# Kernel tuning notes

Hardware: AMD Instinct MI355X
Metric: run time of the kernel (lower is better)

The kernel has to match this reference:

```python
import jax, jax.numpy as jnp
import numpy as np

EPS = 1e-5
B, S, P = 2, 512, 4096
TD, SD, H, ED = 512, 384, 8, 32
HD = TD // H


def _ln(x, g, b):
    m = jnp.mean(x, axis=-1, keepdims=True)
    v = jnp.var(x, axis=-1, keepdims=True)
    return (x - m) * jax.lax.rsqrt(v + EPS) * g + b


def setup_inputs() -> dict:
    key = jax.random.key(0)
    ks = iter(jax.random.split(key, 24))

    def lin(din, dout):
        W = jax.random.normal(next(ks), (din, dout), jnp.float32) / np.sqrt(din)
        b = jnp.zeros((dout,), jnp.float32)
        return W, b

    Wq, bq = lin(TD, TD)
    Wk, bk = lin(SD, TD)
    Wv, bv = lin(SD, TD)
    Wo, bo = lin(TD, TD)
    W1, b1 = lin(TD, 4 * TD)
    W2, b2 = lin(4 * TD, TD)
    edge_emb = jax.random.normal(next(ks), (H, ED), jnp.float32)
    ep_w = jax.random.normal(next(ks), (ED,), jnp.float32) / np.sqrt(ED)
    ep_b = jnp.zeros((), jnp.float32)

    return dict(
        text_features=jax.random.normal(next(ks), (B, S, TD), jnp.float32),
        shape_features=jax.random.normal(next(ks), (B, P, SD), jnp.float32),
        tn_g=jnp.ones((TD,), jnp.float32), tn_b=jnp.zeros((TD,), jnp.float32),
        sn_g=jnp.ones((SD,), jnp.float32), sn_b=jnp.zeros((SD,), jnp.float32),
        Wq=Wq, bq=bq, Wk=Wk, bk=bk, Wv=Wv, bv=bv,
        edge_emb=edge_emb, ep_w=ep_w, ep_b=ep_b,
        Wo=Wo, bo=bo,
        on_g=jnp.ones((TD,), jnp.float32), on_b=jnp.zeros((TD,), jnp.float32),
        W1=W1, b1=b1, W2=W2, b2=b2,
        fn_g=jnp.ones((TD,), jnp.float32), fn_b=jnp.zeros((TD,), jnp.float32),
    )


def reference(text_features, shape_features, tn_g, tn_b, sn_g, sn_b,
              Wq, bq, Wk, bk, Wv, bv, edge_emb, ep_w, ep_b, Wo, bo,
              on_g, on_b, W1, b1, W2, b2, fn_g, fn_b):
    b, n, _ = text_features.shape
    tn = _ln(text_features, tn_g, tn_b)
    sn = _ln(shape_features, sn_g, sn_b)
    residual = text_features

    # [b, h, n, d] projections
    q = (tn @ Wq + bq).reshape(b, n, H, HD).transpose(0, 2, 1, 3)
    k = (sn @ Wk + bk).reshape(b, -1, H, HD).transpose(0, 2, 1, 3)
    v = (sn @ Wv + bv).reshape(b, -1, H, HD).transpose(0, 2, 1, 3)

    scale = HD ** -0.5
    base_attn = jnp.einsum('bhid,bhjd->bhij', q, k) * scale  # [b,h,n,p]

    # edge_attn[:,h] = base_attn[:,h,:,:,None] * edge_emb[h]; then Linear(ED,1)+LeakyReLU.
    # Algebraically: score = leaky_relu(base_attn * (edge_emb @ ep_w) + ep_b)
    s = edge_emb @ ep_w  # [H] per-head scalar
    edge_scores = jax.nn.leaky_relu(base_attn * s[None, :, None, None] + ep_b, 0.2)

    attn = jax.nn.softmax(base_attn + edge_scores, axis=-1)
    out = jnp.einsum('bhij,bhjd->bhid', attn, v)
    out = out.transpose(0, 2, 1, 3).reshape(b, n, TD)
    out = out @ Wo + bo
    out = _ln(residual + out, on_g, on_b)

    ffn = jax.nn.gelu(out @ W1 + b1, approximate=False) @ W2 + b2
    out = _ln(out + ffn, fn_g, fn_b)
    return out, attn
```

## Files before the change

### kernel.cpp

```cpp
#include <hip/hip_runtime.h>
#include <math.h>

#define B_  2
#define S_  512
#define P_  4096
#define TD_ 512
#define SD_ 384
#define H_  8
#define HD_ 64
#define FF_ 2048

typedef _Float16 half8 __attribute__((ext_vector_type(8)));
typedef _Float16 half4 __attribute__((ext_vector_type(4)));
typedef float floatx4 __attribute__((ext_vector_type(4)));

__global__ __launch_bounds__(256) void wtrans_all_kernel(
    const float* __restrict__ s0p, const float* __restrict__ s1p,
    const float* __restrict__ s2p, const float* __restrict__ s3p,
    const float* __restrict__ s4p, const float* __restrict__ s5p,
    _Float16* __restrict__ d0p, _Float16* __restrict__ d1p,
    _Float16* __restrict__ d2p, _Float16* __restrict__ d3p,
    _Float16* __restrict__ d4p, _Float16* __restrict__ d5p)
{
    __shared__ float ts[32][33];
    int id = blockIdx.x;
    const float* src; _Float16* dst; int K, N, t, nlog;
    if (id < 256)       { src=s0p; dst=d0p; K=512;  N=512;  t=id;       nlog=4; }
    else if (id < 448)  { src=s1p; dst=d1p; K=384;  N=512;  t=id-256;   nlog=4; }
    else if (id < 640)  { src=s2p; dst=d2p; K=384;  N=512;  t=id-448;   nlog=4; }
    else if (id < 896)  { src=s3p; dst=d3p; K=512;  N=512;  t=id-640;   nlog=4; }
    else if (id < 1920) { src=s4p; dst=d4p; K=512;  N=2048; t=id-896;   nlog=6; }
    else                { src=s5p; dst=d5p; K=2048; N=512;  t=id-1920;  nlog=4; }
    int n0 = (t & ((1 << nlog) - 1)) << 5;
    int k0 = (t >> nlog) << 5;
    int tid = threadIdx.x;
#pragma unroll
    for (int i = 0; i < 4; ++i) {
        int e = i * 256 + tid;
        int kk = e >> 5, nn = e & 31;
        ts[kk][nn] = src[(size_t)(k0 + kk) * N + n0 + nn];
    }
    __syncthreads();
#pragma unroll
    for (int i = 0; i < 4; ++i) {
        int e = i * 256 + tid;
        int nn = e >> 5, kk = e & 31;
        dst[(size_t)(n0 + nn) * K + k0 + kk] = (_Float16)ts[kk][nn];
    }
}

__device__ __forceinline__ float2 block_sum2(float a, float b) {
    for (int off = 32; off > 0; off >>= 1) {
        a += __shfl_down(a, off);
        b += __shfl_down(b, off);
    }
    __shared__ float sa[8], sb[8];
    int w = threadIdx.x >> 6;
    if ((threadIdx.x & 63) == 0) { sa[w] = a; sb[w] = b; }
    __syncthreads();
    int nw = blockDim.x >> 6;
    float ta = 0.f, tb = 0.f;
    for (int i = 0; i < nw; ++i) { ta += sa[i]; tb += sb[i]; }
    __syncthreads();
    return make_float2(ta, tb);
}

__global__ __launch_bounds__(256) void ln_both_kernel(
    const float* __restrict__ text, const float* __restrict__ shape,
    const float* __restrict__ tn_g, const float* __restrict__ tn_b,
    const float* __restrict__ sn_g, const float* __restrict__ sn_b,
    _Float16* __restrict__ tn_h, _Float16* __restrict__ sn_h)
{
    int row = blockIdx.x;
    const float* xr; const float* g; const float* be; _Float16* yr; int D;
    if (row < 1024) {
        D = 512; xr = text + (size_t)row * 512; g = tn_g; be = tn_b;
        yr = tn_h + (size_t)row * 512;
    } else {
        int r2 = row - 1024;
        D = 384; xr = shape + (size_t)r2 * 384; g = sn_g; be = sn_b;
        yr = sn_h + (size_t)r2 * 384;
    }
    float s = 0.f, s2 = 0.f;
    for (int i = threadIdx.x; i < D; i += 256) {
        float v = xr[i]; s += v; s2 += v * v;
    }
    float2 r = block_sum2(s, s2);
    float mean = r.x / (float)D;
    float var  = r.y / (float)D - mean * mean;
    float rstd = rsqrtf(var + 1e-5f);
    for (int i = threadIdx.x; i < D; i += 256)
        yr[i] = (_Float16)((xr[i] - mean) * rstd * g[i] + be[i]);
}

__global__ __launch_bounds__(256) void ln_add_kernel(
    const float* __restrict__ a, const float* __restrict__ c, int np, int cstride,
    const float* __restrict__ g, const float* __restrict__ be,
    float* __restrict__ yf, _Float16* __restrict__ yh, int D)
{
    int row = blockIdx.x;
    const float* ar = a + (size_t)row * D;
    const float* cr = c + (size_t)row * D;
    float s = 0.f, s2 = 0.f;
    for (int i = threadIdx.x; i < D; i += 256) {
        float v = ar[i];
        for (int t = 0; t < np; ++t) v += cr[(size_t)t * cstride + i];
        s += v; s2 += v * v;
    }
    float2 rd = block_sum2(s, s2);
    float mean = rd.x / (float)D;
    float var  = rd.y / (float)D - mean * mean;
    float rstd = rsqrtf(var + 1e-5f);
    for (int i = threadIdx.x; i < D; i += 256) {
        float v = ar[i];
        for (int t = 0; t < np; ++t) v += cr[(size_t)t * cstride + i];
        float o = (v - mean) * rstd * g[i] + be[i];
        if (yf) yf[(size_t)row * D + i] = o;
        if (yh) yh[(size_t)row * D + i] = (_Float16)o;
    }
}

template<int ACT, int OUTF, int OUTH, int SPLITK>
__global__ __launch_bounds__(256) void gemm_f16_kernel(
    const _Float16* __restrict__ A, const _Float16* __restrict__ Bt,
    const float* __restrict__ bias, float* __restrict__ Cf,
    _Float16* __restrict__ Ch, int M, int N, int K)
{
    __shared__ _Float16 As[128 * 40];
    __shared__ _Float16 Bs[128 * 40];
    int tid = threadIdx.x;
    int bm = blockIdx.y * 128, bn = blockIdx.x * 128;
    int wave = tid >> 6, lane = tid & 63, quad = lane >> 4, r = lane & 15;
    int mh = (wave & 1) * 64, nh = (wave >> 1) * 64;

    floatx4 acc[4][4];
    floatx4 zz = {0.f, 0.f, 0.f, 0.f};
#pragma unroll
    for (int i = 0; i < 4; ++i)
#pragma unroll
        for (int j = 0; j < 4; ++j) acc[i][j] = zz;

    int srow = tid >> 2;
    int sko  = (tid & 3) * 8;

    int ksplit = (SPLITK > 1) ? blockIdx.z : 0;
    int kbeg = ksplit * (K / SPLITK);
    int kend = kbeg + K / SPLITK;

    for (int k0 = kbeg; k0 < kend; k0 += 32) {
#pragma unroll
        for (int i = 0; i < 2; ++i) {
            int row = i * 64 + srow;
            *(half8*)&As[row * 40 + sko] = *(const half8*)(A  + (size_t)(bm + row) * K + k0 + sko);
            *(half8*)&Bs[row * 40 + sko] = *(const half8*)(Bt + (size_t)(bn + row) * K + k0 + sko);
        }
        __syncthreads();
        half8 af[4], bf[4];
#pragma unroll
        for (int t = 0; t < 4; ++t) {
            af[t] = *(const half8*)&As[(mh + t * 16 + r) * 40 + quad * 8];
            bf[t] = *(const half8*)&Bs[(nh + t * 16 + r) * 40 + quad * 8];
        }
#pragma unroll
        for (int i = 0; i < 4; ++i)
#pragma unroll
            for (int j = 0; j < 4; ++j)
                acc[i][j] = __builtin_amdgcn_mfma_f32_16x16x32_f16(af[i], bf[j], acc[i][j], 0, 0, 0);
        __syncthreads();
    }

#pragma unroll
    for (int j = 0; j < 4; ++j) {
        int col = bn + nh + j * 16 + r;
        float bv = (SPLITK == 1 || ksplit == 0) ? bias[col] : 0.f;
#pragma unroll
        for (int i = 0; i < 4; ++i) {
#pragma unroll
            for (int g = 0; g < 4; ++g) {
                int row = bm + mh + i * 16 + quad * 4 + g;
                float v = acc[i][j][g] + bv;
                if (ACT) v = 0.5f * v * (1.0f + erff(v * 0.70710678118654752f));
                if (OUTF) Cf[(size_t)ksplit * M * N + (size_t)row * N + col] = v;
                if (OUTH) Ch[(size_t)row * N + col] = (_Float16)v;
            }
        }
    }
}

__global__ __launch_bounds__(256) void qkv_gemm_kernel(
    const _Float16* __restrict__ tn, const _Float16* __restrict__ sn,
    const _Float16* __restrict__ Wqt, const _Float16* __restrict__ Wkt,
    const _Float16* __restrict__ Wvt,
    const float* __restrict__ bq, const float* __restrict__ bk,
    const float* __restrict__ bv,
    _Float16* __restrict__ Qh, _Float16* __restrict__ Kh, _Float16* __restrict__ Vth)
{
    __shared__ _Float16 As[128 * 40];
    __shared__ _Float16 Bs[128 * 40];
    int by = blockIdx.y;
    const _Float16* A; const _Float16* Bt; const float* bias; _Float16* out;
    int K, bm, vt;
    if (by < 8)       { A = tn; Bt = Wqt; bias = bq; K = 512; bm = by * 128;        vt = 0; out = Qh;  }
    else if (by < 72) { A = sn; Bt = Wkt; bias = bk; K = 384; bm = (by - 8) * 128;  vt = 0; out = Kh;  }
    else              { A = sn; Bt = Wvt; bias = bv; K = 384; bm = (by - 72) * 128; vt = 1; out = Vth; }
    int bn = blockIdx.x * 128;
    int tid = threadIdx.x;
    int wave = tid >> 6, lane = tid & 63, quad = lane >> 4, r = lane & 15;
    int mh = (wave & 1) * 64, nh = (wave >> 1) * 64;

    floatx4 acc[4][4];
    floatx4 zz = {0.f, 0.f, 0.f, 0.f};
#pragma unroll
    for (int i = 0; i < 4; ++i)
#pragma unroll
        for (int j = 0; j < 4; ++j) acc[i][j] = zz;

    int srow = tid >> 2;
    int sko  = (tid & 3) * 8;

    for (int k0 = 0; k0 < K; k0 += 32) {
#pragma unroll
        for (int i = 0; i < 2; ++i) {
            int row = i * 64 + srow;
            *(half8*)&As[row * 40 + sko] = *(const half8*)(A  + (size_t)(bm + row) * K + k0 + sko);
            *(half8*)&Bs[row * 40 + sko] = *(const half8*)(Bt + (size_t)(bn + row) * K + k0 + sko);
        }
        __syncthreads();
        half8 af[4], bf[4];
#pragma unroll
        for (int t = 0; t < 4; ++t) {
            af[t] = *(const half8*)&As[(mh + t * 16 + r) * 40 + quad * 8];
            bf[t] = *(const half8*)&Bs[(nh + t * 16 + r) * 40 + quad * 8];
        }
#pragma unroll
        for (int i = 0; i < 4; ++i)
#pragma unroll
            for (int j = 0; j < 4; ++j)
                acc[i][j] = __builtin_amdgcn_mfma_f32_16x16x32_f16(af[i], bf[j], acc[i][j], 0, 0, 0);
        __syncthreads();
    }

#pragma unroll
    for (int j = 0; j < 4; ++j) {
        int col = bn + nh + j * 16 + r;
        float bvv = bias[col];
#pragma unroll
        for (int i = 0; i < 4; ++i) {
#pragma unroll
            for (int g = 0; g < 4; ++g) {
                int row = bm + mh + i * 16 + quad * 4 + g;
                float v = acc[i][j][g] + bvv;
                if (!vt) {
                    out[(size_t)row * 512 + col] = (_Float16)v;
                } else {
                    int bb = row >> 12, pp = row & 4095;
                    int hh = col >> 6,  dd = col & 63;
                    out[((size_t)((bb * 8 + hh) * 64 + dd)) * 4096 + pp] = (_Float16)v;
                }
            }
        }
    }
}

__global__ __launch_bounds__(256) void score_stats_kernel(
    const _Float16* __restrict__ Qh, const _Float16* __restrict__ Kh,
    const float* __restrict__ edge_emb, const float* __restrict__ ep_w,
    const float* __restrict__ ep_b, float2* __restrict__ part)
{
    __shared__ _Float16 Qs[128 * 72];
    __shared__ _Float16 Ks[128 * 72];
    __shared__ float mred[2][128];
    __shared__ float sred[2][128];
    int p0 = blockIdx.x * 128, s0 = blockIdx.y * 128;
    int bh = blockIdx.z, h = bh & 7, b = bh >> 3;
    int tid = threadIdx.x;
    int wave = tid >> 6, lane = tid & 63, quad = lane >> 4, r = lane & 15;
    int mh = (wave & 1) * 64, nh = (wave >> 1) * 64;

#pragma unroll
    for (int i = 0; i < 4; ++i) {
        int row = i * 32 + (tid >> 3);
        int ko  = (tid & 7) * 8;
        *(half8*)&Qs[row * 72 + ko] = *(const half8*)(Qh + (size_t)(b * S_ + s0 + row) * TD_ + h * HD_ + ko);
        *(half8*)&Ks[row * 72 + ko] = *(const half8*)(Kh + (size_t)(b * P_ + p0 + row) * TD_ + h * HD_ + ko);
    }
    float s_h = 0.f;
#pragma unroll
    for (int e = 0; e < 32; ++e) s_h += edge_emb[h * 32 + e] * ep_w[e];
    float epbv = ep_b[0];
    __syncthreads();

    floatx4 acc[4][4];
    floatx4 zz = {0.f, 0.f, 0.f, 0.f};
#pragma unroll
    for (int i = 0; i < 4; ++i)
#pragma unroll
        for (int j = 0; j < 4; ++j) acc[i][j] = zz;

#pragma unroll
    for (int c = 0; c < 2; ++c) {
        half8 af[4], bf[4];
#pragma unroll
        for (int t = 0; t < 4; ++t) {
            af[t] = *(const half8*)&Qs[(mh + t * 16 + r) * 72 + c * 32 + quad * 8];
            bf[t] = *(const half8*)&Ks[(nh + t * 16 + r) * 72 + c * 32 + quad * 8];
        }
#pragma unroll
        for (int i = 0; i < 4; ++i)
#pragma unroll
            for (int j = 0; j < 4; ++j)
                acc[i][j] = __builtin_amdgcn_mfma_f32_16x16x32_f16(af[i], bf[j], acc[i][j], 0, 0, 0);
    }

    const float scale = 0.125f;
#pragma unroll
    for (int i = 0; i < 4; ++i)
#pragma unroll
        for (int j = 0; j < 4; ++j)
#pragma unroll
            for (int g = 0; g < 4; ++g) {
                float base = acc[i][j][g] * scale;
                float t = fmaf(base, s_h, epbv);
                float e = (t >= 0.f) ? t : 0.2f * t;
                acc[i][j][g] = base + e;
            }

    float mv[16], sv[16];
#pragma unroll
    for (int i = 0; i < 4; ++i)
#pragma unroll
        for (int g = 0; g < 4; ++g)
            mv[i * 4 + g] = fmaxf(fmaxf(acc[i][0][g], acc[i][1][g]),
                                  fmaxf(acc[i][2][g], acc[i][3][g]));
#pragma unroll
    for (int mask = 1; mask <= 8; mask <<= 1)
#pragma unroll
        for (int t = 0; t < 16; ++t)
            mv[t] = fmaxf(mv[t], __shfl_xor(mv[t], mask));
#pragma unroll
    for (int i = 0; i < 4; ++i)
#pragma unroll
        for (int g = 0; g < 4; ++g) {
            float s = 0.f;
#pragma unroll
            for (int j = 0; j < 4; ++j) s += __expf(acc[i][j][g] - mv[i * 4 + g]);
            sv[i * 4 + g] = s;
        }
#pragma unroll
    for (int mask = 1; mask <= 8; mask <<= 1)
#pragma unroll
        for (int t = 0; t < 16; ++t)
            sv[t] += __shfl_xor(sv[t], mask);

    if (r == 0) {
#pragma unroll
        for (int i = 0; i < 4; ++i)
#pragma unroll
            for (int g = 0; g < 4; ++g) {
                int row = mh + i * 16 + quad * 4 + g;
                mred[wave >> 1][row] = mv[i * 4 + g];
                sred[wave >> 1][row] = sv[i * 4 + g];
            }
    }
    __syncthreads();
    if (tid < 128) {
        float m0 = mred[0][tid], m1 = mred[1][tid];
        float m = fmaxf(m0, m1);
        float s = sred[0][tid] * __expf(m0 - m) + sred[1][tid] * __expf(m1 - m);
        part[(size_t)blockIdx.x * (B_ * H_ * S_) + (size_t)bh * S_ + s0 + tid] = make_float2(m, s);
    }
}

__global__ __launch_bounds__(256) void attn_pv_kernel(
    const _Float16* __restrict__ Qh, const _Float16* __restrict__ Kh,
    const _Float16* __restrict__ Vt,
    const float* __restrict__ edge_emb, const float* __restrict__ ep_w,
    const float* __restrict__ ep_b, const float2* __restrict__ part,
    float* __restrict__ attn, float* __restrict__ ctx_part)
{
    __shared__ _Float16 Qs[32 * 72];
    __shared__ _Float16 Ks[128 * 72];
    __shared__ _Float16 Vs[64 * 136];
    __shared__ _Float16 As[32 * 136];
    __shared__ float2 ms_sh[32];

    int s0 = blockIdx.x * 32;
    int split = blockIdx.y;
    int bh = blockIdx.z, h = bh & 7, b = bh >> 3;
    int tid = threadIdx.x;
    int wave = tid >> 6, lane = tid & 63, quad = lane >> 4, r = lane & 15;

    {
        int row = tid >> 3, ko = (tid & 7) * 8;
        *(half8*)&Qs[row * 72 + ko] =
            *(const half8*)(Qh + (size_t)(b * S_ + s0 + row) * TD_ + h * HD_ + ko);
    }
    if (tid < 32) {
        int base = bh * S_ + s0 + tid;
        float2 v = part[base];
        float m = v.x, l = v.y;
#pragma unroll
        for (int t = 1; t < 32; ++t) {
            float2 p = part[(size_t)t * (B_ * H_ * S_) + base];
            float nm = fmaxf(m, p.x);
            l = l * __expf(m - nm) + p.y * __expf(p.x - nm);
            m = nm;
        }
        ms_sh[tid] = make_float2(m, 1.0f / l);
    }

    float s_h = 0.f;
#pragma unroll
    for (int e = 0; e < 32; ++e) s_h += edge_emb[h * 32 + e] * ep_w[e];
    float epbv = ep_b[0];

    floatx4 zz = {0.f, 0.f, 0.f, 0.f};
    floatx4 accpv[2];
    accpv[0] = zz; accpv[1] = zz;

    for (int pc = 0; pc < 1024; pc += 128) {
        int pg = split * 1024 + pc;
        __syncthreads();
#pragma unroll
        for (int ii = 0; ii < 4; ++ii) {
            int e = ii * 256 + tid;
            int row = e >> 3, ko = (e & 7) * 8;
            *(half8*)&Ks[row * 72 + ko] =
                *(const half8*)(Kh + (size_t)(b * P_ + pg + row) * TD_ + h * HD_ + ko);
        }
#pragma unroll
        for (int ii = 0; ii < 4; ++ii) {
            int e = ii * 256 + tid;
            int row = e >> 4, po = (e & 15) * 8;
            *(half8*)&Vs[row * 136 + po] =
                *(const half8*)(Vt + ((size_t)bh * 64 + row) * (size_t)P_ + pg + po);
        }
        __syncthreads();

        floatx4 accs[2][2];
        accs[0][0] = zz; accs[0][1] = zz; accs[1][0] = zz; accs[1][1] = zz;
#pragma unroll
        for (int c = 0; c < 2; ++c) {
            half8 aq[2], bk[2];
#pragma unroll
            for (int i = 0; i < 2; ++i)
                aq[i] = *(const half8*)&Qs[(i * 16 + r) * 72 + c * 32 + quad * 8];
#pragma unroll
            for (int j = 0; j < 2; ++j)
                bk[j] = *(const half8*)&Ks[(wave * 32 + j * 16 + r) * 72 + c * 32 + quad * 8];
#pragma unroll
            for (int i = 0; i < 2; ++i)
#pragma unroll
                for (int j = 0; j < 2; ++j)
                    accs[i][j] = __builtin_amdgcn_mfma_f32_16x16x32_f16(aq[i], bk[j], accs[i][j], 0, 0, 0);
        }

        const float scale = 0.125f;
#pragma unroll
        for (int i = 0; i < 2; ++i)
#pragma unroll
            for (int j = 0; j < 2; ++j) {
                int colp = wave * 32 + j * 16 + r;
#pragma unroll
                for (int g = 0; g < 4; ++g) {
                    int srow = i * 16 + quad * 4 + g;
                    float base = accs[i][j][g] * scale;
                    float t = fmaf(base, s_h, epbv);
                    float e = (t >= 0.f) ? t : 0.2f * t;
                    float z = base + e;
                    float2 ms = ms_sh[srow];
                    float p = __expf(z - ms.x) * ms.y;
                    attn[((size_t)bh * S_ + s0 + srow) * P_ + pg + colp] = p;
                    As[srow * 136 + colp] = (_Float16)p;
                }
            }
        __syncthreads();

#pragma unroll
        for (int c = 0; c < 4; ++c) {
            half8 bv = *(const half8*)&Vs[(wave * 16 + r) * 136 + c * 32 + quad * 8];
#pragma unroll
            for (int i2 = 0; i2 < 2; ++i2) {
                half8 ap = *(const half8*)&As[(i2 * 16 + r) * 136 + c * 32 + quad * 8];
                accpv[i2] = __builtin_amdgcn_mfma_f32_16x16x32_f16(ap, bv, accpv[i2], 0, 0, 0);
            }
        }
    }

    float* dst = ctx_part + (size_t)split * (1024 * 512);
#pragma unroll
    for (int i2 = 0; i2 < 2; ++i2)
#pragma unroll
        for (int g = 0; g < 4; ++g) {
            int srow = s0 + i2 * 16 + quad * 4 + g;
            int d = wave * 16 + r;
            dst[(size_t)(b * S_ + srow) * TD_ + h * HD_ + d] = accpv[i2][g];
        }
}

__global__ __launch_bounds__(256) void sumcast_kernel(
    const float4* __restrict__ src, _Float16* __restrict__ dst, int n4)
{
    int i = blockIdx.x * 256 + threadIdx.x;
    if (i < n4) {
        float4 a = src[i];
        float4 bq = src[i + 131072];
        float4 c = src[i + 262144];
        float4 d = src[i + 393216];
        float4 v = make_float4(a.x + bq.x + c.x + d.x, a.y + bq.y + c.y + d.y,
                               a.z + bq.z + c.z + d.z, a.w + bq.w + c.w + d.w);
        half4 hv = { (_Float16)v.x, (_Float16)v.y, (_Float16)v.z, (_Float16)v.w };
        *(half4*)&dst[(size_t)i * 4] = hv;
    }
}

extern "C" void kernel_launch(void* const* d_in, const int* in_sizes, int n_in,
                              void* d_out, int out_size, void* d_ws, size_t ws_size,
                              hipStream_t stream) {
    const float* text  = (const float*)d_in[0];
    const float* shape = (const float*)d_in[1];
    const float* tn_g  = (const float*)d_in[2];
    const float* tn_b  = (const float*)d_in[3];
    const float* sn_g  = (const float*)d_in[4];
    const float* sn_b  = (const float*)d_in[5];
    const float* Wq    = (const float*)d_in[6];
    const float* bq    = (const float*)d_in[7];
    const float* Wk    = (const float*)d_in[8];
    const float* bk    = (const float*)d_in[9];
    const float* Wv    = (const float*)d_in[10];
    const float* bv    = (const float*)d_in[11];
    const float* edge  = (const float*)d_in[12];
    const float* epw   = (const float*)d_in[13];
    const float* epb   = (const float*)d_in[14];
    const float* Wo    = (const float*)d_in[15];
    const float* bo    = (const float*)d_in[16];
    const float* on_g  = (const float*)d_in[17];
    const float* on_b  = (const float*)d_in[18];
    const float* W1    = (const float*)d_in[19];
    const float* b1    = (const float*)d_in[20];
    const float* W2    = (const float*)d_in[21];
    const float* b2    = (const float*)d_in[22];
    const float* fn_g  = (const float*)d_in[23];
    const float* fn_b  = (const float*)d_in[24];

    float* out_f  = (float*)d_out;
    float* attn_f = out_f + (size_t)B_ * S_ * TD_;

    char* w = (char*)d_ws;
    _Float16* tn_h   = (_Float16*)w; w += (size_t)1024 * 512 * 2;
    _Float16* sn_h   = (_Float16*)w; w += (size_t)8192 * 384 * 2;
    _Float16* Q_h    = (_Float16*)w; w += (size_t)1024 * 512 * 2;
    _Float16* K_h    = (_Float16*)w; w += (size_t)8192 * 512 * 2;
    _Float16* Vt_h   = (_Float16*)w; w += (size_t)16 * 64 * 4096 * 2;
    _Float16* ctx_h  = (_Float16*)w; w += (size_t)1024 * 512 * 2;
    _Float16* out1_h = (_Float16*)w; w += (size_t)1024 * 512 * 2;
    _Float16* h1_h   = (_Float16*)w; w += (size_t)1024 * 2048 * 2;
    _Float16* Wqt    = (_Float16*)w; w += (size_t)512 * 512 * 2;
    _Float16* Wkt    = (_Float16*)w; w += (size_t)512 * 384 * 2;
    _Float16* Wvt    = (_Float16*)w; w += (size_t)512 * 384 * 2;
    _Float16* Wot    = (_Float16*)w; w += (size_t)512 * 512 * 2;
    _Float16* W1t    = (_Float16*)w; w += (size_t)2048 * 512 * 2;
    _Float16* W2t    = (_Float16*)w; w += (size_t)512 * 2048 * 2;
    float*    tmp    = (float*)w;    w += (size_t)1024 * 512 * 4;
    float*    out1_f = (float*)w;    w += (size_t)1024 * 512 * 4;
    float*    ctx_part = (float*)w;  w += (size_t)4 * 1024 * 512 * 4;

    float2* part = (float2*)sn_h;

    wtrans_all_kernel<<<2944, 256, 0, stream>>>(Wq, Wk, Wv, Wo, W1, W2,
                                                Wqt, Wkt, Wvt, Wot, W1t, W2t);

    ln_both_kernel<<<1024 + 8192, 256, 0, stream>>>(text, shape, tn_g, tn_b, sn_g, sn_b, tn_h, sn_h);

    qkv_gemm_kernel<<<dim3(4, 136), 256, 0, stream>>>(tn_h, sn_h, Wqt, Wkt, Wvt,
                                                      bq, bk, bv, Q_h, K_h, Vt_h);

    score_stats_kernel<<<dim3(P_ / 128, S_ / 128, B_ * H_), 256, 0, stream>>>(
        Q_h, K_h, edge, epw, epb, part);
    attn_pv_kernel<<<dim3(S_ / 32, 4, B_ * H_), 256, 0, stream>>>(
        Q_h, K_h, Vt_h, edge, epw, epb, part, attn_f, ctx_part);
    sumcast_kernel<<<dim3(512), 256, 0, stream>>>((const float4*)ctx_part, ctx_h, 131072);

    gemm_f16_kernel<0,1,0,1><<<dim3(4, 8), 256, 0, stream>>>(ctx_h, Wot, bo, tmp, nullptr, 1024, 512, 512);
    ln_add_kernel<<<B_ * S_, 256, 0, stream>>>(text, tmp, 1, 0, on_g, on_b, out1_f, out1_h, TD_);

    gemm_f16_kernel<1,0,1,1><<<dim3(16, 8), 256, 0, stream>>>(out1_h, W1t, b1, nullptr, h1_h, 1024, 2048, 512);
    gemm_f16_kernel<0,1,0,4><<<dim3(4, 8, 4), 256, 0, stream>>>(h1_h, W2t, b2, ctx_part, nullptr, 1024, 512, 2048);
    ln_add_kernel<<<B_ * S_, 256, 0, stream>>>(out1_f, ctx_part, 4, 1024 * 512, fn_g, fn_b, out_f, nullptr, TD_);
}
```

Measured before the change: 366.8 us.

## Merge prep kernels, register-prefetch GEMM tiles, widen attention split, split-K Wo GEMM

Merges the weight-transpose and layernorm kernels into one launch. Adds register double-buffering of global loads in the GEMM, QKV and attention-PV kernels so the next tile is fetched while the current one is computed. Doubles the attention P-split from 4 to 8 for more parallelism and sums 8 partials, uses nontemporal stores for the large attn output, applies split-K 4 to the Wo GEMM, and specializes ln_add for D=512. This trades more partial-sum traffic and register pressure for better latency hiding and occupancy.

```diff
diff --git a/kernel.cpp b/kernel.cpp
--- a/kernel.cpp
+++ b/kernel.cpp
@@ -13,41 +13,6 @@
 typedef _Float16 half8 __attribute__((ext_vector_type(8)));
 typedef _Float16 half4 __attribute__((ext_vector_type(4)));
 typedef float floatx4 __attribute__((ext_vector_type(4)));
-
-__global__ __launch_bounds__(256) void wtrans_all_kernel(
-    const float* __restrict__ s0p, const float* __restrict__ s1p,
-    const float* __restrict__ s2p, const float* __restrict__ s3p,
-    const float* __restrict__ s4p, const float* __restrict__ s5p,
-    _Float16* __restrict__ d0p, _Float16* __restrict__ d1p,
-    _Float16* __restrict__ d2p, _Float16* __restrict__ d3p,
-    _Float16* __restrict__ d4p, _Float16* __restrict__ d5p)
-{
-    __shared__ float ts[32][33];
-    int id = blockIdx.x;
-    const float* src; _Float16* dst; int K, N, t, nlog;
-    if (id < 256)       { src=s0p; dst=d0p; K=512;  N=512;  t=id;       nlog=4; }
-    else if (id < 448)  { src=s1p; dst=d1p; K=384;  N=512;  t=id-256;   nlog=4; }
-    else if (id < 640)  { src=s2p; dst=d2p; K=384;  N=512;  t=id-448;   nlog=4; }
-    else if (id < 896)  { src=s3p; dst=d3p; K=512;  N=512;  t=id-640;   nlog=4; }
-    else if (id < 1920) { src=s4p; dst=d4p; K=512;  N=2048; t=id-896;   nlog=6; }
-    else                { src=s5p; dst=d5p; K=2048; N=512;  t=id-1920;  nlog=4; }
-    int n0 = (t & ((1 << nlog) - 1)) << 5;
-    int k0 = (t >> nlog) << 5;
-    int tid = threadIdx.x;
-#pragma unroll
-    for (int i = 0; i < 4; ++i) {
-        int e = i * 256 + tid;
-        int kk = e >> 5, nn = e & 31;
-        ts[kk][nn] = src[(size_t)(k0 + kk) * N + n0 + nn];
-    }
-    __syncthreads();
-#pragma unroll
-    for (int i = 0; i < 4; ++i) {
-        int e = i * 256 + tid;
-        int nn = e >> 5, kk = e & 31;
-        dst[(size_t)(n0 + nn) * K + k0 + kk] = (_Float16)ts[kk][nn];
-    }
-}
 
 __device__ __forceinline__ float2 block_sum2(float a, float b) {
     for (int off = 32; off > 0; off >>= 1) {
@@ -65,13 +30,47 @@
     return make_float2(ta, tb);
 }
 
-__global__ __launch_bounds__(256) void ln_both_kernel(
+__global__ __launch_bounds__(256) void prep_kernel(
+    const float* __restrict__ s0p, const float* __restrict__ s1p,
+    const float* __restrict__ s2p, const float* __restrict__ s3p,
+    const float* __restrict__ s4p, const float* __restrict__ s5p,
+    _Float16* __restrict__ d0p, _Float16* __restrict__ d1p,
+    _Float16* __restrict__ d2p, _Float16* __restrict__ d3p,
+    _Float16* __restrict__ d4p, _Float16* __restrict__ d5p,
     const float* __restrict__ text, const float* __restrict__ shape,
     const float* __restrict__ tn_g, const float* __restrict__ tn_b,
     const float* __restrict__ sn_g, const float* __restrict__ sn_b,
     _Float16* __restrict__ tn_h, _Float16* __restrict__ sn_h)
 {
-    int row = blockIdx.x;
+    __shared__ float ts[32][33];
+    int id = blockIdx.x;
+    int tid = threadIdx.x;
+    if (id < 2944) {
+        const float* src; _Float16* dst; int K, N, t, nlog;
+        if (id < 256)       { src=s0p; dst=d0p; K=512;  N=512;  t=id;       nlog=4; }
+        else if (id < 448)  { src=s1p; dst=d1p; K=384;  N=512;  t=id-256;   nlog=4; }
+        else if (id < 640)  { src=s2p; dst=d2p; K=384;  N=512;  t=id-448;   nlog=4; }
+        else if (id < 896)  { src=s3p; dst=d3p; K=512;  N=512;  t=id-640;   nlog=4; }
+        else if (id < 1920) { src=s4p; dst=d4p; K=512;  N=2048; t=id-896;   nlog=6; }
+        else                { src=s5p; dst=d5p; K=2048; N=512;  t=id-1920;  nlog=4; }
+        int n0 = (t & ((1 << nlog) - 1)) << 5;
+        int k0 = (t >> nlog) << 5;
+#pragma unroll
+        for (int i = 0; i < 4; ++i) {
+            int e = i * 256 + tid;
+            int kk = e >> 5, nn = e & 31;
+            ts[kk][nn] = src[(size_t)(k0 + kk) * N + n0 + nn];
+        }
+        __syncthreads();
+#pragma unroll
+        for (int i = 0; i < 4; ++i) {
+            int e = i * 256 + tid;
+            int nn = e >> 5, kk = e & 31;
+            dst[(size_t)(n0 + nn) * K + k0 + kk] = (_Float16)ts[kk][nn];
+        }
+        return;
+    }
+    int row = id - 2944;
     const float* xr; const float* g; const float* be; _Float16* yr; int D;
     if (row < 1024) {
         D = 512; xr = text + (size_t)row * 512; g = tn_g; be = tn_b;
@@ -82,42 +81,39 @@
         yr = sn_h + (size_t)r2 * 384;
     }
     float s = 0.f, s2 = 0.f;
-    for (int i = threadIdx.x; i < D; i += 256) {
+    for (int i = tid; i < D; i += 256) {
         float v = xr[i]; s += v; s2 += v * v;
     }
     float2 r = block_sum2(s, s2);
     float mean = r.x / (float)D;
     float var  = r.y / (float)D - mean * mean;
     float rstd = rsqrtf(var + 1e-5f);
-    for (int i = threadIdx.x; i < D; i += 256)
+    for (int i = tid; i < D; i += 256)
         yr[i] = (_Float16)((xr[i] - mean) * rstd * g[i] + be[i]);
 }
 
 __global__ __launch_bounds__(256) void ln_add_kernel(
     const float* __restrict__ a, const float* __restrict__ c, int np, int cstride,
     const float* __restrict__ g, const float* __restrict__ be,
-    float* __restrict__ yf, _Float16* __restrict__ yh, int D)
+    float* __restrict__ yf, _Float16* __restrict__ yh)
 {
     int row = blockIdx.x;
-    const float* ar = a + (size_t)row * D;
-    const float* cr = c + (size_t)row * D;
-    float s = 0.f, s2 = 0.f;
-    for (int i = threadIdx.x; i < D; i += 256) {
-        float v = ar[i];
-        for (int t = 0; t < np; ++t) v += cr[(size_t)t * cstride + i];
-        s += v; s2 += v * v;
-    }
-    float2 rd = block_sum2(s, s2);
-    float mean = rd.x / (float)D;
-    float var  = rd.y / (float)D - mean * mean;
+    int i0 = threadIdx.x, i1 = threadIdx.x + 256;
+    const float* ar = a + (size_t)row * 512;
+    const float* cr = c + (size_t)row * 512;
+    float v0 = ar[i0], v1 = ar[i1];
+    for (int t = 0; t < np; ++t) {
+        v0 += cr[(size_t)t * cstride + i0];
+        v1 += cr[(size_t)t * cstride + i1];
+    }
+    float2 rd = block_sum2(v0 + v1, v0 * v0 + v1 * v1);
+    float mean = rd.x / 512.f;
+    float var  = rd.y / 512.f - mean * mean;
     float rstd = rsqrtf(var + 1e-5f);
-    for (int i = threadIdx.x; i < D; i += 256) {
-        float v = ar[i];
-        for (int t = 0; t < np; ++t) v += cr[(size_t)t * cstride + i];
-        float o = (v - mean) * rstd * g[i] + be[i];
-        if (yf) yf[(size_t)row * D + i] = o;
-        if (yh) yh[(size_t)row * D + i] = (_Float16)o;
-    }
+    float o0 = (v0 - mean) * rstd * g[i0] + be[i0];
+    float o1 = (v1 - mean) * rstd * g[i1] + be[i1];
+    if (yf) { yf[(size_t)row * 512 + i0] = o0; yf[(size_t)row * 512 + i1] = o1; }
+    if (yh) { yh[(size_t)row * 512 + i0] = (_Float16)o0; yh[(size_t)row * 512 + i1] = (_Float16)o1; }
 }
 
 template<int ACT, int OUTF, int OUTH, int SPLITK>
@@ -147,14 +143,28 @@
     int kbeg = ksplit * (K / SPLITK);
     int kend = kbeg + K / SPLITK;
 
+    const _Float16* Ap0 = A  + (size_t)(bm + srow) * K + sko;
+    const _Float16* Ap1 = A  + (size_t)(bm + srow + 64) * K + sko;
+    const _Float16* Bp0 = Bt + (size_t)(bn + srow) * K + sko;
+    const _Float16* Bp1 = Bt + (size_t)(bn + srow + 64) * K + sko;
+
+    half8 ra0 = *(const half8*)(Ap0 + kbeg);
+    half8 ra1 = *(const half8*)(Ap1 + kbeg);
+    half8 rb0 = *(const half8*)(Bp0 + kbeg);
+    half8 rb1 = *(const half8*)(Bp1 + kbeg);
+
     for (int k0 = kbeg; k0 < kend; k0 += 32) {
-#pragma unroll
-        for (int i = 0; i < 2; ++i) {
-            int row = i * 64 + srow;
-            *(half8*)&As[row * 40 + sko] = *(const half8*)(A  + (size_t)(bm + row) * K + k0 + sko);
-            *(half8*)&Bs[row * 40 + sko] = *(const half8*)(Bt + (size_t)(bn + row) * K + k0 + sko);
-        }
-        __syncthreads();
+        *(half8*)&As[srow * 40 + sko]        = ra0;
+        *(half8*)&As[(srow + 64) * 40 + sko] = ra1;
+        *(half8*)&Bs[srow * 40 + sko]        = rb0;
+        *(half8*)&Bs[(srow + 64) * 40 + sko] = rb1;
+        __syncthreads();
+        if (k0 + 32 < kend) {
+            ra0 = *(const half8*)(Ap0 + k0 + 32);
+            ra1 = *(const half8*)(Ap1 + k0 + 32);
+            rb0 = *(const half8*)(Bp0 + k0 + 32);
+            rb1 = *(const half8*)(Bp1 + k0 + 32);
+        }
         half8 af[4], bf[4];
 #pragma unroll
         for (int t = 0; t < 4; ++t) {
@@ -218,14 +228,28 @@
     int srow = tid >> 2;
     int sko  = (tid & 3) * 8;
 
+    const _Float16* Ap0 = A  + (size_t)(bm + srow) * K + sko;
+    const _Float16* Ap1 = A  + (size_t)(bm + srow + 64) * K + sko;
+    const _Float16* Bp0 = Bt + (size_t)(bn + srow) * K + sko;
+    const _Float16* Bp1 = Bt + (size_t)(bn + srow + 64) * K + sko;
+
+    half8 ra0 = *(const half8*)(Ap0);
+    half8 ra1 = *(const half8*)(Ap1);
+    half8 rb0 = *(const half8*)(Bp0);
+    half8 rb1 = *(const half8*)(Bp1);
+
     for (int k0 = 0; k0 < K; k0 += 32) {
-#pragma unroll
-        for (int i = 0; i < 2; ++i) {
-            int row = i * 64 + srow;
-            *(half8*)&As[row * 40 + sko] = *(const half8*)(A  + (size_t)(bm + row) * K + k0 + sko);
-            *(half8*)&Bs[row * 40 + sko] = *(const half8*)(Bt + (size_t)(bn + row) * K + k0 + sko);
-        }
-        __syncthreads();
+        *(half8*)&As[srow * 40 + sko]        = ra0;
+        *(half8*)&As[(srow + 64) * 40 + sko] = ra1;
+        *(half8*)&Bs[srow * 40 + sko]        = rb0;
+        *(half8*)&Bs[(srow + 64) * 40 + sko] = rb1;
+        __syncthreads();
+        if (k0 + 32 < K) {
+            ra0 = *(const half8*)(Ap0 + k0 + 32);
+            ra1 = *(const half8*)(Ap1 + k0 + 32);
+            rb0 = *(const half8*)(Bp0 + k0 + 32);
+            rb1 = *(const half8*)(Bp1 + k0 + 32);
+        }
         half8 af[4], bf[4];
 #pragma unroll
         for (int t = 0; t < 4; ++t) {
@@ -414,48 +438,60 @@
     for (int e = 0; e < 32; ++e) s_h += edge_emb[h * 32 + e] * ep_w[e];
     float epbv = ep_b[0];
 
+    const _Float16* Kbase = Kh + (size_t)b * P_ * TD_ + h * HD_;
+    const _Float16* Vbase = Vt + (size_t)bh * 64 * P_;
+
+    int pg0 = split * 512;
+    half8 rk[4], rv[4];
+#pragma unroll
+    for (int ii = 0; ii < 4; ++ii) {
+        int e = ii * 256 + tid;
+        rk[ii] = *(const half8*)(Kbase + (size_t)(pg0 + (e >> 3)) * TD_ + (e & 7) * 8);
+        rv[ii] = *(const half8*)(Vbase + (size_t)(e >> 4) * P_ + pg0 + (e & 15) * 8);
+    }
+
     floatx4 zz = {0.f, 0.f, 0.f, 0.f};
     floatx4 accpv[2];
     accpv[0] = zz; accpv[1] = zz;
-
-    for (int pc = 0; pc < 1024; pc += 128) {
-        int pg = split * 1024 + pc;
-        __syncthreads();
+    const float scale = 0.125f;
+
+    for (int c = 0; c < 4; ++c) {
+        int pg = pg0 + c * 128;
 #pragma unroll
         for (int ii = 0; ii < 4; ++ii) {
             int e = ii * 256 + tid;
-            int row = e >> 3, ko = (e & 7) * 8;
-            *(half8*)&Ks[row * 72 + ko] =
-                *(const half8*)(Kh + (size_t)(b * P_ + pg + row) * TD_ + h * HD_ + ko);
-        }
-#pragma unroll
-        for (int ii = 0; ii < 4; ++ii) {
-            int e = ii * 256 + tid;
-            int row = e >> 4, po = (e & 15) * 8;
-            *(half8*)&Vs[row * 136 + po] =
-                *(const half8*)(Vt + ((size_t)bh * 64 + row) * (size_t)P_ + pg + po);
-        }
-        __syncthreads();
+            *(half8*)&Ks[(e >> 3) * 72 + (e & 7) * 8]  = rk[ii];
+            *(half8*)&Vs[(e >> 4) * 136 + (e & 15) * 8] = rv[ii];
+        }
+        __syncthreads();
+        if (c < 3) {
+            int pn = pg + 128;
+#pragma unroll
+            for (int ii = 0; ii < 4; ++ii) {
+                int e = ii * 256 + tid;
+                rk[ii] = *(const half8*)(Kbase + (size_t)(pn + (e >> 3)) * TD_ + (e & 7) * 8);
+                rv[ii] = *(const half8*)(Vbase + (size_t)(e >> 4) * P_ + pn + (e & 15) * 8);
+            }
+        }
 
         floatx4 accs[2][2];
         accs[0][0] = zz; accs[0][1] = zz; accs[1][0] = zz; accs[1][1] = zz;
 #pragma unroll
-        for (int c = 0; c < 2; ++c) {
-            half8 aq[2], bk[2];
+        for (int c2 = 0; c2 < 2; ++c2) {
+            half8 aq[2], bk2[2];
 #pragma unroll
             for (int i = 0; i < 2; ++i)
-                aq[i] = *(const half8*)&Qs[(i * 16 + r) * 72 + c * 32 + quad * 8];
+                aq[i] = *(const half8*)&Qs[(i * 16 + r) * 72 + c2 * 32 + quad * 8];
 #pragma unroll
             for (int j = 0; j < 2; ++j)
-                bk[j] = *(const half8*)&Ks[(wave * 32 + j * 16 + r) * 72 + c * 32 + quad * 8];
+                bk2[j] = *(const half8*)&Ks[(wave * 32 + j * 16 + r) * 72 + c2 * 32 + quad * 8];
 #pragma unroll
             for (int i = 0; i < 2; ++i)
 #pragma unroll
                 for (int j = 0; j < 2; ++j)
-                    accs[i][j] = __builtin_amdgcn_mfma_f32_16x16x32_f16(aq[i], bk[j], accs[i][j], 0, 0, 0);
-        }
-
-        const float scale = 0.125f;
+                    accs[i][j] = __builtin_amdgcn_mfma_f32_16x16x32_f16(aq[i], bk2[j], accs[i][j], 0, 0, 0);
+        }
+
 #pragma unroll
         for (int i = 0; i < 2; ++i)
 #pragma unroll
@@ -470,21 +506,22 @@
                     float z = base + e;
                     float2 ms = ms_sh[srow];
                     float p = __expf(z - ms.x) * ms.y;
-                    attn[((size_t)bh * S_ + s0 + srow) * P_ + pg + colp] = p;
+                    __builtin_nontemporal_store(p, &attn[((size_t)bh * S_ + s0 + srow) * P_ + pg + colp]);
                     As[srow * 136 + colp] = (_Float16)p;
                 }
             }
         __syncthreads();
 
 #pragma unroll
-        for (int c = 0; c < 4; ++c) {
-            half8 bv = *(const half8*)&Vs[(wave * 16 + r) * 136 + c * 32 + quad * 8];
+        for (int cc = 0; cc < 4; ++cc) {
+            half8 bv = *(const half8*)&Vs[(wave * 16 + r) * 136 + cc * 32 + quad * 8];
 #pragma unroll
             for (int i2 = 0; i2 < 2; ++i2) {
-                half8 ap = *(const half8*)&As[(i2 * 16 + r) * 136 + c * 32 + quad * 8];
+                half8 ap = *(const half8*)&As[(i2 * 16 + r) * 136 + cc * 32 + quad * 8];
                 accpv[i2] = __builtin_amdgcn_mfma_f32_16x16x32_f16(ap, bv, accpv[i2], 0, 0, 0);
             }
         }
+        __syncthreads();
     }
 
     float* dst = ctx_part + (size_t)split * (1024 * 512);
@@ -503,12 +540,12 @@
 {
     int i = blockIdx.x * 256 + threadIdx.x;
     if (i < n4) {
-        float4 a = src[i];
-        float4 bq = src[i + 131072];
-        float4 c = src[i + 262144];
-        float4 d = src[i + 393216];
-        float4 v = make_float4(a.x + bq.x + c.x + d.x, a.y + bq.y + c.y + d.y,
-                               a.z + bq.z + c.z + d.z, a.w + bq.w + c.w + d.w);
+        float4 v = src[i];
+#pragma unroll
+        for (int t = 1; t < 8; ++t) {
+            float4 p = src[i + t * 131072];
+            v.x += p.x; v.y += p.y; v.z += p.z; v.w += p.w;
+        }
         half4 hv = { (_Float16)v.x, (_Float16)v.y, (_Float16)v.z, (_Float16)v.w };
         *(half4*)&dst[(size_t)i * 4] = hv;
     }
@@ -561,30 +598,28 @@
     _Float16* Wot    = (_Float16*)w; w += (size_t)512 * 512 * 2;
     _Float16* W1t    = (_Float16*)w; w += (size_t)2048 * 512 * 2;
     _Float16* W2t    = (_Float16*)w; w += (size_t)512 * 2048 * 2;
-    float*    tmp    = (float*)w;    w += (size_t)1024 * 512 * 4;
     float*    out1_f = (float*)w;    w += (size_t)1024 * 512 * 4;
-    float*    ctx_part = (float*)w;  w += (size_t)4 * 1024 * 512 * 4;
+    float*    ctx_part = (float*)w;  w += (size_t)8 * 1024 * 512 * 4;
 
     float2* part = (float2*)sn_h;
 
-    wtrans_all_kernel<<<2944, 256, 0, stream>>>(Wq, Wk, Wv, Wo, W1, W2,
-                                                Wqt, Wkt, Wvt, Wot, W1t, W2t);
-
-    ln_both_kernel<<<1024 + 8192, 256, 0, stream>>>(text, shape, tn_g, tn_b, sn_g, sn_b, tn_h, sn_h);
+    prep_kernel<<<2944 + 1024 + 8192, 256, 0, stream>>>(
+        Wq, Wk, Wv, Wo, W1, W2, Wqt, Wkt, Wvt, Wot, W1t, W2t,
+        text, shape, tn_g, tn_b, sn_g, sn_b, tn_h, sn_h);
 
     qkv_gemm_kernel<<<dim3(4, 136), 256, 0, stream>>>(tn_h, sn_h, Wqt, Wkt, Wvt,
                                                       bq, bk, bv, Q_h, K_h, Vt_h);
 
     score_stats_kernel<<<dim3(P_ / 128, S_ / 128, B_ * H_), 256, 0, stream>>>(
         Q_h, K_h, edge, epw, epb, part);
-    attn_pv_kernel<<<dim3(S_ / 32, 4, B_ * H_), 256, 0, stream>>>(
+    attn_pv_kernel<<<dim3(S_ / 32, 8, B_ * H_), 256, 0, stream>>>(
         Q_h, K_h, Vt_h, edge, epw, epb, part, attn_f, ctx_part);
     sumcast_kernel<<<dim3(512), 256, 0, stream>>>((const float4*)ctx_part, ctx_h, 131072);
 
-    gemm_f16_kernel<0,1,0,1><<<dim3(4, 8), 256, 0, stream>>>(ctx_h, Wot, bo, tmp, nullptr, 1024, 512, 512);
-    ln_add_kernel<<<B_ * S_, 256, 0, stream>>>(text, tmp, 1, 0, on_g, on_b, out1_f, out1_h, TD_);
+    gemm_f16_kernel<0,1,0,4><<<dim3(4, 8, 4), 256, 0, stream>>>(ctx_h, Wot, bo, ctx_part, nullptr, 1024, 512, 512);
+    ln_add_kernel<<<B_ * S_, 256, 0, stream>>>(text, ctx_part, 4, 1024 * 512, on_g, on_b, out1_f, out1_h);
 
     gemm_f16_kernel<1,0,1,1><<<dim3(16, 8), 256, 0, stream>>>(out1_h, W1t, b1, nullptr, h1_h, 1024, 2048, 512);
     gemm_f16_kernel<0,1,0,4><<<dim3(4, 8, 4), 256, 0, stream>>>(h1_h, W2t, b2, ctx_part, nullptr, 1024, 512, 2048);
-    ln_add_kernel<<<B_ * S_, 256, 0, stream>>>(out1_f, ctx_part, 4, 1024 * 512, fn_g, fn_b, out_f, nullptr, TD_);
-}
+    ln_add_kernel<<<B_ * S_, 256, 0, stream>>>(out1_f, ctx_part, 4, 1024 * 512, fn_g, fn_b, out_f, nullptr);
+}
```

Result: faster. 356.2 us (-2.9%).
